# Optimization experiments

Hardware: AMD Instinct MI355X
Metric: run time of the kernel (lower is better)

The kernel has to match this reference:

```python
import jax, jax.numpy as jnp
import numpy as np

K = 16  # number of nearest neighbors (excluding self)


def setup_inputs() -> dict:
    key = jax.random.key(0)
    kp, kf = jax.random.split(key)
    points = jax.random.normal(kp, (8, 4096, 3), dtype=jnp.float32)    # (B, P, D)
    features = jax.random.normal(kf, (8, 4096, 64), dtype=jnp.float32)  # (B, P, C)
    return {"points": points, "features": features}


def reference(points, features):
    # small_d distance path (D <= 4): (a - b)^2 summed over coord dim
    # a_: (B, P, D, 1), b_: (B, 1, D, P) -> dist: (B, P, P)
    a_ = points[:, :, :, None]
    b_ = jnp.transpose(points, (0, 2, 1))[:, None, :, :]
    dist = jnp.sum(jnp.square(a_ - b_), axis=2)
    # top-(k+1) of negative distance, drop self (first column)
    _, idx = jax.lax.top_k(-dist, K + 1)          # (B, P, K+1)
    idx = idx[:, :, 1:]                            # (B, P, K)
    # gather neighbor features with batch_dims=1
    knn_fts = jax.vmap(lambda f, i: f[i])(features, idx)   # (B, P, K, C)
    # tile center features along K and concat on last axis -> (B, P, K, 2C)
    center = jnp.broadcast_to(features[:, :, None, :], knn_fts.shape)
    return jnp.concatenate([center, knn_fts], axis=-1)
```

## Files before the change

kernel.cpp:

```cpp
#include <hip/hip_runtime.h>


#define BATCH 8
#define NPTS 4096
#define FDIM 64
#define KNN 16
#define QPB 64
#define NSUB 16
#define CPL (NPTS / NSUB)
#define THREADS (QPB * NSUB)
#define LCAP 48
#define HSTRIDE 129
#define BUCKC 920
#define NSEL 17

__global__ __launch_bounds__(THREADS, 4)
void knn_kernel(const float* __restrict__ points,
                const float* __restrict__ features,
                float* __restrict__ out) {
    __shared__ __align__(16) unsigned char smem[35584];
    unsigned* hist = (unsigned*)smem;
    unsigned long long* slist = (unsigned long long*)smem;
    unsigned* ubnd = (unsigned*)(smem + 33024);
    unsigned* scnt = (unsigned*)(smem + 33280);
    unsigned short* sidx = (unsigned short*)(smem + 33536);

    const int tid = threadIdx.x;
    const int b = blockIdx.x >> 6;
    const int qbase = (blockIdx.x & 63) << 6;
    const float* pb = points + (size_t)b * NPTS * 3;

    const int q = tid & (QPB - 1);
    const int sub = tid >> 6;
    const int qg0 = qbase + q;

    for (int i = tid; i < QPB * HSTRIDE; i += THREADS) hist[i] = 0;
    if (tid < QPB) scnt[tid] = 0;

    const float qx = pb[qg0 * 3 + 0];
    const float qy = pb[qg0 * 3 + 1];
    const float qz = pb[qg0 * 3 + 2];

    const int jbase = __builtin_amdgcn_readfirstlane(sub) * CPL;
    const float* __restrict__ ps = pb + (size_t)jbase * 3;
    const int hrow = q * HSTRIDE;

    __syncthreads();

#pragma unroll 4
    for (int jj = 0; jj < CPL; ++jj) {
        const float px = ps[jj * 3 + 0];
        const float py = ps[jj * 3 + 1];
        const float pz = ps[jj * 3 + 2];
        const float dx = qx - px;
        const float dy = qy - py;
        const float dz = qz - pz;
        const float d = __fadd_rn(__fadd_rn(__fmul_rn(dx, dx), __fmul_rn(dy, dy)),
                                  __fmul_rn(dz, dz));
        int bk = (int)(__float_as_uint(d) >> 20) - BUCKC;
        bk = min(127, max(0, bk));
        atomicAdd(&hist[hrow + bk], 1u);
    }
    __syncthreads();

    if (tid < QPB) {
        unsigned c = 0;
        int bsel = 0;
#pragma unroll 8
        for (int bb = 0; bb < 128; ++bb) {
            c += hist[tid * HSTRIDE + bb];
            bsel += (c < NSEL);
        }
        ubnd[tid] = (bsel >= 127) ? 0x7f800000u
                                  : ((unsigned)(bsel + 1 + BUCKC) << 20);
    }
    __syncthreads();

    const unsigned ub = ubnd[q];
    const unsigned pbase2 = (unsigned)q;
#pragma unroll 4
    for (int jj = 0; jj < CPL; ++jj) {
        const float px = ps[jj * 3 + 0];
        const float py = ps[jj * 3 + 1];
        const float pz = ps[jj * 3 + 2];
        const float dx = qx - px;
        const float dy = qy - py;
        const float dz = qz - pz;
        const float d = __fadd_rn(__fadd_rn(__fmul_rn(dx, dx), __fmul_rn(dy, dy)),
                                  __fmul_rn(dz, dz));
        const unsigned dbits = __float_as_uint(d);
        if (dbits < ub) {
            const unsigned pos = atomicAdd(&scnt[q], 1u);
            if (pos < LCAP)
                slist[pos * QPB + pbase2] =
                    (((unsigned long long)dbits) << 32) | (unsigned)(jbase + jj);
        }
    }
    __syncthreads();

    if (tid < QPB) {
        const int c = min((int)scnt[tid], LCAP);
        unsigned long long prev = 0ULL;
        for (int s = 0; s < NSEL; ++s) {
            unsigned long long best = ~0ULL;
            for (int i = 0; i < c; ++i) {
                const unsigned long long k = slist[i * QPB + tid];
                if (k >= prev && k < best) best = k;
            }
            if (s > 0)
                sidx[tid * KNN + (s - 1)] = (unsigned short)(best & 0xFFFFULL);
            prev = best + 1ULL;
        }
    }
    __syncthreads();

    const float* __restrict__ fb = features + (size_t)b * NPTS * FDIM;
    float* __restrict__ ob = out + (size_t)b * NPTS * (KNN * 2 * FDIM);
#pragma unroll 2
    for (int it = 0; it < 32; ++it) {
        const int flat = it * THREADS + tid;
        const int c4 = flat & 31;
        const int k = (flat >> 5) & 15;
        const int qq = flat >> 9;
        const int qg = qbase + qq;
        const int row = (c4 < 16) ? qg : (int)sidx[qq * KNN + k];
        const float4 v = *(const float4*)(fb + (size_t)row * FDIM + ((c4 & 15) << 2));
        *(float4*)(ob + (((size_t)(qg * KNN + k)) << 7) + (c4 << 2)) = v;
    }
}

extern "C" void kernel_launch(void* const* d_in, const int* in_sizes, int n_in,
                              void* d_out, int out_size, void* d_ws, size_t ws_size,
                              hipStream_t stream) {
    const float* points = (const float*)d_in[0];
    const float* features = (const float*)d_in[1];
    float* out = (float*)d_out;
    const int grid = BATCH * (NPTS / QPB);
    knn_kernel<<<dim3(grid), dim3(THREADS), 0, stream>>>(points, features, out);
}
```

Baseline: 341.9 us.

## Parallelize top-k selection via rank counting across all threads, add nontemporal stores

Replaces the serial 17-pass selection, which ran on only 64 threads, with a rank-counting scheme. All 16 sub-threads per query each compute the rank of candidate entries in parallel and scatter them into place. The filter distance now uses FMA with a one-bucket wider bound, while exact non-FMA distances are kept for ordering; the candidate cap grows to 64. The output gather switches to nontemporal stores to reduce cache pollution from the large streaming write. The wider bound admits more candidates per query, and overflow past the cap could drop true neighbors.

Measured after the change: 334.0 us. 1.02x faster.

```diff
diff --git a/kernel.cpp b/kernel.cpp
--- a/kernel.cpp
+++ b/kernel.cpp
@@ -1,5 +1,7 @@
 #include <hip/hip_runtime.h>
 
+
+typedef float f32x4 __attribute__((ext_vector_type(4)));
 
 #define BATCH 8
 #define NPTS 4096
@@ -9,7 +11,7 @@
 #define NSUB 16
 #define CPL (NPTS / NSUB)
 #define THREADS (QPB * NSUB)
-#define LCAP 48
+#define LCAP 64
 #define HSTRIDE 129
 #define BUCKC 920
 #define NSEL 17
@@ -55,8 +57,7 @@
         const float dx = qx - px;
         const float dy = qy - py;
         const float dz = qz - pz;
-        const float d = __fadd_rn(__fadd_rn(__fmul_rn(dx, dx), __fmul_rn(dy, dy)),
-                                  __fmul_rn(dz, dz));
+        const float d = __fmaf_rn(dx, dx, __fmaf_rn(dy, dy, __fmul_rn(dz, dz)));
         int bk = (int)(__float_as_uint(d) >> 20) - BUCKC;
         bk = min(127, max(0, bk));
         atomicAdd(&hist[hrow + bk], 1u);
@@ -71,13 +72,12 @@
             c += hist[tid * HSTRIDE + bb];
             bsel += (c < NSEL);
         }
-        ubnd[tid] = (bsel >= 127) ? 0x7f800000u
-                                  : ((unsigned)(bsel + 1 + BUCKC) << 20);
+        ubnd[tid] = (bsel + 1 >= 127) ? 0x7f800000u
+                                      : ((unsigned)(bsel + 2 + BUCKC) << 20);
     }
     __syncthreads();
 
     const unsigned ub = ubnd[q];
-    const unsigned pbase2 = (unsigned)q;
 #pragma unroll 4
     for (int jj = 0; jj < CPL; ++jj) {
         const float px = ps[jj * 3 + 0];
@@ -86,30 +86,28 @@
         const float dx = qx - px;
         const float dy = qy - py;
         const float dz = qz - pz;
-        const float d = __fadd_rn(__fadd_rn(__fmul_rn(dx, dx), __fmul_rn(dy, dy)),
-                                  __fmul_rn(dz, dz));
-        const unsigned dbits = __float_as_uint(d);
-        if (dbits < ub) {
+        const float d = __fmaf_rn(dx, dx, __fmaf_rn(dy, dy, __fmul_rn(dz, dz)));
+        if (__float_as_uint(d) < ub) {
+            const float de = __fadd_rn(__fadd_rn(__fmul_rn(dx, dx), __fmul_rn(dy, dy)),
+                                       __fmul_rn(dz, dz));
             const unsigned pos = atomicAdd(&scnt[q], 1u);
             if (pos < LCAP)
-                slist[pos * QPB + pbase2] =
-                    (((unsigned long long)dbits) << 32) | (unsigned)(jbase + jj);
+                slist[pos * QPB + q] =
+                    (((unsigned long long)__float_as_uint(de)) << 32)
+                    | (unsigned)(jbase + jj);
         }
     }
     __syncthreads();
 
-    if (tid < QPB) {
-        const int c = min((int)scnt[tid], LCAP);
-        unsigned long long prev = 0ULL;
-        for (int s = 0; s < NSEL; ++s) {
-            unsigned long long best = ~0ULL;
-            for (int i = 0; i < c; ++i) {
-                const unsigned long long k = slist[i * QPB + tid];
-                if (k >= prev && k < best) best = k;
-            }
-            if (s > 0)
-                sidx[tid * KNN + (s - 1)] = (unsigned short)(best & 0xFFFFULL);
-            prev = best + 1ULL;
+    {
+        const int c = min((int)scnt[q], LCAP);
+        for (int slot = sub; slot < c; slot += NSUB) {
+            const unsigned long long mykey = slist[slot * QPB + q];
+            int rank = 0;
+            for (int m = 0; m < c; ++m)
+                rank += (slist[m * QPB + q] < mykey);
+            if (rank >= 1 && rank <= KNN)
+                sidx[q * KNN + (rank - 1)] = (unsigned short)(mykey & 0xFFFFULL);
         }
     }
     __syncthreads();
@@ -124,8 +122,9 @@
         const int qq = flat >> 9;
         const int qg = qbase + qq;
         const int row = (c4 < 16) ? qg : (int)sidx[qq * KNN + k];
-        const float4 v = *(const float4*)(fb + (size_t)row * FDIM + ((c4 & 15) << 2));
-        *(float4*)(ob + (((size_t)(qg * KNN + k)) << 7) + (c4 << 2)) = v;
+        const f32x4 v = *(const f32x4*)(fb + (size_t)row * FDIM + ((c4 & 15) << 2));
+        __builtin_nontemporal_store(
+            v, (f32x4*)(ob + (((size_t)(qg * KNN + k)) << 7) + (c4 << 2)));
     }
 }
 
```
